# Kernel optimization log

Measured on AMD Instinct MI355X. Metric: run time of the kernel, lower is better.

## Reference

```python
import jax, jax.numpy as jnp
import numpy as np
from jax import lax

B, S, H, DK = 8192, 12, 8, 64
DM = H * DK  # d_model = 512


def setup_inputs() -> dict:
    key = jax.random.key(0)
    ks = jax.random.split(key, 7)
    query = jax.random.normal(ks[0], (B, S, DM), jnp.float32)
    key_t = jax.random.normal(ks[1], (B, S, DM), jnp.float32)
    value = jax.random.normal(ks[2], (B, S, DM), jnp.float32)
    mask = jnp.ones((B, S, S), jnp.int32)
    # conv1d12: Conv1d(12, 12, 3, 1, 1) -> weight [out_ch=12, in_ch=12, k=3]
    conv_w = jax.random.normal(ks[3], (S, S, 3), jnp.float32) * 0.1
    conv_b = jax.random.normal(ks[4], (S,), jnp.float32) * 0.1
    # final output projection linears[-1]: Linear(512, 512)
    W_out = jax.random.normal(ks[5], (DM, DM), jnp.float32) * (1.0 / np.sqrt(DM))
    b_out = jax.random.normal(ks[6], (DM,), jnp.float32) * 0.01
    return {"query": query, "key": key_t, "value": value, "mask": mask,
            "conv_w": conv_w, "conv_b": conv_b, "W_out": W_out, "b_out": b_out}


def _neighbor_sums(nodes):
    # nodes: [H, B, S, DK]. convo12 pattern == 3-tap sum over head index with zero ends:
    #   s0 = n0+n1; s_i = n_{i-1}+n_i+n_{i+1} (i=1..6); s7 = n6+n7
    p = jnp.pad(nodes, ((1, 1), (0, 0), (0, 0), (0, 0)))
    return p[:-2] + p[1:-1] + p[2:]  # [H, B, S, DK]


def _conv12(x, w, b):
    # x: [N, S, DK] -> conv over length DK with S channels, kernel 3, pad 1
    y = lax.conv_general_dilated(x, w, window_strides=(1,), padding=[(1, 1)],
                                 dimension_numbers=("NCH", "OIH", "NCH"))
    return y + b[None, :, None]


def reference(query, key, value, mask, conv_w, conv_b, W_out, b_out):
    def split_heads(x):
        # torch.split(x, d_k, -1) over 8 heads -> [H, B, S, DK]
        return jnp.moveaxis(x.reshape(B, S, H, DK), 2, 0)

    def conv_all(x):
        s = _neighbor_sums(split_heads(x)).reshape(H * B, S, DK)
        return _conv12(s, conv_w, conv_b).reshape(H, B, S, DK)

    # reunion: stack heads at dim 1 -> [B, H, S, DK]
    q = jnp.moveaxis(conv_all(query), 0, 1)
    k = jnp.moveaxis(conv_all(key), 0, 1)
    v = jnp.moveaxis(conv_all(value), 0, 1)

    scores = jnp.einsum("bhqd,bhkd->bhqk", q, k) / np.sqrt(DK).astype(np.float32)
    # mask.unsqueeze(1): [B,1,S,S]; masked_fill(mask==0, -1e9)
    scores = jnp.where(mask[:, None, :, :] == 0, jnp.float32(-1e9), scores)
    p = jax.nn.softmax(scores, axis=-1)  # dropout = identity (eval mode)
    x = jnp.einsum("bhqk,bhkd->bhqd", p, v)
    x = jnp.moveaxis(x, 1, 2).reshape(B, S, DM)  # transpose(1,2).view
    return x @ W_out.T + b_out
```

## Files before the change

kernel.cpp:

```cpp
#include <hip/hip_runtime.h>
#include <hip/hip_bf16.h>
#include <math.h>

#define NB 8192
#define NS 12
#define NH 8
#define NDK 64
#define NDM 512

typedef __attribute__((ext_vector_type(8))) short bf16x8;
typedef __attribute__((ext_vector_type(4))) float f32x4;

static __device__ __forceinline__ short f2bfb(float x) {
    __hip_bfloat16 h = __float2bfloat16(x);
    return *(short*)&h;
}
static __device__ __forceinline__ float bfb2f(short s) {
    unsigned u = ((unsigned)(unsigned short)s) << 16;
    return __uint_as_float(u);
}

__global__ __launch_bounds__(512) void wcvt_kernel(const float* __restrict__ W,
                                                   __hip_bfloat16* __restrict__ Wb) {
    int i = blockIdx.x * 512 + threadIdx.x;
    Wb[i] = __float2bfloat16(W[i]);
}

__global__ __launch_bounds__(256) void conv4_kernel(
    const float* __restrict__ gq, const float* __restrict__ gk, const float* __restrict__ gv,
    const float* __restrict__ gcw, const float* __restrict__ gcb,
    short* __restrict__ qc, short* __restrict__ kc, short* __restrict__ vc)
{
    __shared__ __align__(16) float wt[3][12][12];
    __shared__ __align__(16) float bconv[12];

    const int tid = threadIdx.x;
    for (int i = tid; i < 444; i += 256) {
        if (i < 432) {
            int t = i / 144, rem = i - t * 144;
            int s2 = rem / 12, s = rem - s2 * 12;
            wt[t][s2][s] = gcw[s * 36 + s2 * 3 + t];
        } else {
            bconv[i - 432] = gcb[i - 432];
        }
    }
    __syncthreads();

    const int t3   = blockIdx.y;
    const int lane = tid & 63;
    const int w    = tid >> 6;
    const int d4   = lane & 15;
    const int d0   = d4 * 4;
    const int h    = ((w & 1) << 2) + (lane >> 4);
    const int b    = blockIdx.x * 2 + (w >> 1);

    const float* src = (t3 == 0) ? gq : (t3 == 1) ? gk : gv;
    const float* xb  = src + (size_t)b * (NS * NDM);

    const float fm = (h > 0) ? 1.f : 0.f;
    const float fp = (h < 7) ? 1.f : 0.f;
    const float4* pa = (const float4*)(xb + h * 64 + d0);
    const float4* pm = (const float4*)(xb + (h > 0 ? h - 1 : h) * 64 + d0);
    const float4* pp = (const float4*)(xb + (h < 7 ? h + 1 : h) * 64 + d0);

    f32x4 o[12];
    #pragma unroll
    for (int s = 0; s < 12; ++s) {
        float bs = bconv[s];
        o[s] = (f32x4){bs, bs, bs, bs};
    }

    #pragma unroll 2
    for (int s2 = 0; s2 < 12; ++s2) {
        float4 a  = pa[s2 * 128];
        float4 am = pm[s2 * 128];
        float4 ap = pp[s2 * 128];
        f32x4 ns;
        ns[0] = a.x + am.x * fm + ap.x * fp;
        ns[1] = a.y + am.y * fm + ap.y * fp;
        ns[2] = a.z + am.z * fm + ap.z * fp;
        ns[3] = a.w + am.w * fm + ap.w * fp;

        float prev = __shfl_up(ns[3], 1, 16);   if (d4 == 0)  prev = 0.f;
        float next = __shfl_down(ns[0], 1, 16); if (d4 == 15) next = 0.f;
        f32x4 nsm = {prev, ns[0], ns[1], ns[2]};
        f32x4 nsp = {ns[1], ns[2], ns[3], next};

        #pragma unroll
        for (int tap = 0; tap < 3; ++tap) {
            const f32x4 nv = (tap == 0) ? nsm : (tap == 1) ? ns : nsp;
            #pragma unroll
            for (int G = 0; G < 3; ++G) {
                f32x4 wv = *(const f32x4*)&wt[tap][s2][G * 4];
                o[G * 4 + 0] += nv * wv[0];
                o[G * 4 + 1] += nv * wv[1];
                o[G * 4 + 2] += nv * wv[2];
                o[G * 4 + 3] += nv * wv[3];
            }
        }
    }

    if (t3 < 2) {
        short* dst = ((t3 == 0) ? qc : kc) + ((size_t)b * NH + h) * (NS * NDK) + d0;
        #pragma unroll
        for (int s = 0; s < 12; ++s) {
            short4 v;
            v.x = f2bfb(o[s][0]); v.y = f2bfb(o[s][1]);
            v.z = f2bfb(o[s][2]); v.w = f2bfb(o[s][3]);
            *(short4*)(dst + s * 64) = v;
        }
    } else {
        short* dstb = vc + (((size_t)b * NH + h) * NDK + d0) * NS;
        #pragma unroll
        for (int dd = 0; dd < 4; ++dd) {
            short4* dst = (short4*)(dstb + dd * NS);
            short4 p0, p1, p2;
            p0.x = f2bfb(o[0][dd]); p0.y = f2bfb(o[1][dd]); p0.z = f2bfb(o[2][dd]);  p0.w = f2bfb(o[3][dd]);
            p1.x = f2bfb(o[4][dd]); p1.y = f2bfb(o[5][dd]); p1.z = f2bfb(o[6][dd]);  p1.w = f2bfb(o[7][dd]);
            p2.x = f2bfb(o[8][dd]); p2.y = f2bfb(o[9][dd]); p2.z = f2bfb(o[10][dd]); p2.w = f2bfb(o[11][dd]);
            dst[0] = p0; dst[1] = p1; dst[2] = p2;
        }
    }
}

__global__ __launch_bounds__(512) void attn3_kernel(
    const short* __restrict__ qc, const short* __restrict__ kc, const short* __restrict__ vc,
    const int* __restrict__ gmask, const __hip_bfloat16* __restrict__ Wb,
    const float* __restrict__ gbo, float* __restrict__ gout)
{
    __shared__ __align__(16) short abuf[48 * 520];
    __shared__ __align__(16) short pbuf[NH][16][24];

    const int tid = threadIdx.x;
    const int w   = tid >> 6;
    const int ln  = tid & 63;
    const int rA  = ln & 15, g = ln >> 4;

    const int b0    = blockIdx.x * 4;
    const int bb    = w & 3;
    const int b     = b0 + bb;
    const int hbase = (w >> 2) * 4;

    const int rAr = (rA < 12) ? rA : 0;

    for (int t = 0; t < 4; ++t) {
        const int h = hbase + t;
        const short* qs = qc + ((size_t)b * NH + h) * (NS * NDK);
        const short* ks = kc + ((size_t)b * NH + h) * (NS * NDK);
        bf16x8 aq0 = *(const bf16x8*)(qs + rAr * 64 + g * 8);
        bf16x8 aq1 = *(const bf16x8*)(qs + rAr * 64 + 32 + g * 8);
        bf16x8 bk0 = *(const bf16x8*)(ks + rAr * 64 + g * 8);
        bf16x8 bk1 = *(const bf16x8*)(ks + rAr * 64 + 32 + g * 8);
        f32x4 sc = {0.f, 0.f, 0.f, 0.f};
        sc = __builtin_amdgcn_mfma_f32_16x16x32_bf16(aq0, bk0, sc, 0, 0, 0);
        sc = __builtin_amdgcn_mfma_f32_16x16x32_bf16(aq1, bk1, sc, 0, 0, 0);

        const int kj = rA;
        const int* mrow = gmask + (size_t)b * 144;
        #pragma unroll
        for (int r = 0; r < 4; ++r) {
            int qi = g * 4 + r;
            float s = sc[r] * 0.125f;
            if (kj >= 12) s = -INFINITY;
            else if (qi < 12 && mrow[qi * 12 + kj] == 0) s = -1e9f;
            float m = s;
            #pragma unroll
            for (int off = 1; off < 16; off <<= 1) m = fmaxf(m, __shfl_xor(m, off, 16));
            float e = __expf(s - m);
            float sum = e;
            #pragma unroll
            for (int off = 1; off < 16; off <<= 1) sum += __shfl_xor(sum, off, 16);
            pbuf[w][qi][kj] = f2bfb(e / sum);
        }

        bf16x8 pa = (bf16x8){0, 0, 0, 0, 0, 0, 0, 0};
        if (g < 2) pa = *(const bf16x8*)(&pbuf[w][rA][g * 8]);

        const short* vcr = vc + (((size_t)b * NH + h) * NDK) * NS;
        #pragma unroll
        for (int i = 0; i < 4; ++i) {
            bf16x8 bv = (bf16x8){0, 0, 0, 0, 0, 0, 0, 0};
            if (g < 2) {
                const short* p = vcr + (i * 16 + rA) * NS + g * 8;
                short4 lo = *(const short4*)(p);
                short4 hi = *(const short4*)(p + 4);
                bv[0] = lo.x; bv[1] = lo.y; bv[2] = lo.z; bv[3] = lo.w;
                bv[4] = hi.x; bv[5] = hi.y; bv[6] = hi.z; bv[7] = hi.w;
            }
            f32x4 pv = {0.f, 0.f, 0.f, 0.f};
            pv = __builtin_amdgcn_mfma_f32_16x16x32_bf16(pa, bv, pv, 0, 0, 0);
            #pragma unroll
            for (int r = 0; r < 4; ++r) {
                int qi = g * 4 + r;
                if (qi < 12)
                    abuf[(bb * 12 + qi) * 520 + h * 64 + i * 16 + rA] = f2bfb(pv[r]);
            }
        }
    }
    __syncthreads();

    {
        const short* Ws = (const short*)Wb;
        const int n_lane = w * 64 + rA;
        f32x4 acc[3][4] = {};
        #pragma unroll 4
        for (int kk = 0; kk < 16; ++kk) {
            int k0 = kk * 32 + g * 8;
            bf16x8 af0 = *(const bf16x8*)(abuf + (rA)      * 520 + k0);
            bf16x8 af1 = *(const bf16x8*)(abuf + (16 + rA) * 520 + k0);
            bf16x8 af2 = *(const bf16x8*)(abuf + (32 + rA) * 520 + k0);
            #pragma unroll
            for (int i = 0; i < 4; ++i) {
                bf16x8 bfg = *(const bf16x8*)(Ws + (size_t)(n_lane + i * 16) * NDM + k0);
                acc[0][i] = __builtin_amdgcn_mfma_f32_16x16x32_bf16(af0, bfg, acc[0][i], 0, 0, 0);
                acc[1][i] = __builtin_amdgcn_mfma_f32_16x16x32_bf16(af1, bfg, acc[1][i], 0, 0, 0);
                acc[2][i] = __builtin_amdgcn_mfma_f32_16x16x32_bf16(af2, bfg, acc[2][i], 0, 0, 0);
            }
        }
        float bias[4];
        #pragma unroll
        for (int i = 0; i < 4; ++i) bias[i] = gbo[w * 64 + i * 16 + rA];
        #pragma unroll
        for (int m = 0; m < 3; ++m) {
            #pragma unroll
            for (int i = 0; i < 4; ++i) {
                int n = w * 64 + i * 16 + rA;
                #pragma unroll
                for (int r = 0; r < 4; ++r) {
                    int mg  = m * 16 + g * 4 + r;
                    int bi  = mg / 12, qi = mg - bi * 12;
                    gout[(((size_t)(b0 + bi)) * NS + qi) * NDM + n] = acc[m][i][r] + bias[i];
                }
            }
        }
    }
}

__global__ __launch_bounds__(512) void mha_fused4_kernel(
    const float* __restrict__ gq, const float* __restrict__ gk, const float* __restrict__ gv,
    const int* __restrict__ gmask, const float* __restrict__ gcw, const float* __restrict__ gcb,
    const __hip_bfloat16* __restrict__ Wb, const float* __restrict__ gbo,
    float* __restrict__ gout)
{
    __shared__ __align__(16) float xstage[NS][NDM];
    __shared__ __align__(16) short ovbuf[18432];
    __shared__ __align__(16) float probs[NH][16][16];
    __shared__ __align__(16) float wt[3][12][12];
    __shared__ __align__(16) float bconv[12];

    const int b   = blockIdx.x;
    const int tid = threadIdx.x;
    const int wv  = tid >> 6;
    const int ln  = tid & 63;
    const int h = wv, d = ln;

    if (tid < 432) {
        int t = tid / 144, rem = tid - t * 144;
        int s2 = rem / 12, s = rem - s2 * 12;
        wt[t][s2][s] = gcw[s * 36 + s2 * 3 + t];
    } else if (tid < 444) {
        bconv[tid - 432] = gcb[tid - 432];
    }

    const size_t xoff = (size_t)b * (NS * NDM);
    float vv[12];

    for (int t3 = 0; t3 < 3; ++t3) {
        const float* xb = ((t3 == 0) ? gq : (t3 == 1) ? gk : gv) + xoff;
        {
            const float4* s4 = (const float4*)xb;
            float4* dst4 = (float4*)&xstage[0][0];
            #pragma unroll
            for (int i = 0; i < 3; ++i) dst4[tid + i * 512] = s4[tid + i * 512];
        }
        __syncthreads();

        f32x4 o0 = *(const f32x4*)&bconv[0];
        f32x4 o1 = *(const f32x4*)&bconv[4];
        f32x4 o2 = *(const f32x4*)&bconv[8];
        #pragma unroll 4
        for (int s2 = 0; s2 < 12; ++s2) {
            float c  = xstage[s2][h * 64 + d];
            float cm = (h > 0) ? xstage[s2][(h - 1) * 64 + d] : 0.f;
            float cp = (h < 7) ? xstage[s2][(h + 1) * 64 + d] : 0.f;
            float n0 = c + cm + cp;
            float nm = __shfl_up(n0, 1);   if (d == 0)  nm = 0.f;
            float np = __shfl_down(n0, 1); if (d == 63) np = 0.f;
            const f32x4* w0 = (const f32x4*)&wt[0][s2][0];
            const f32x4* w1 = (const f32x4*)&wt[1][s2][0];
            const f32x4* w2 = (const f32x4*)&wt[2][s2][0];
            o0 += w0[0] * nm + w1[0] * n0 + w2[0] * np;
            o1 += w0[1] * nm + w1[1] * n0 + w2[1] * np;
            o2 += w0[2] * nm + w1[2] * n0 + w2[2] * np;
        }
        if (t3 < 2) {
            __hip_bfloat16* st = (__hip_bfloat16*)(ovbuf + (wv * 2 + t3) * 1152);
            #pragma unroll
            for (int s = 0; s < 4; ++s) st[s * 72 + d]       = __float2bfloat16(o0[s]);
            #pragma unroll
            for (int s = 0; s < 4; ++s) st[(s + 4) * 72 + d] = __float2bfloat16(o1[s]);
            #pragma unroll
            for (int s = 0; s < 4; ++s) st[(s + 8) * 72 + d] = __float2bfloat16(o2[s]);
            __syncthreads();
        } else {
            #pragma unroll
            for (int s = 0; s < 4; ++s) { vv[s] = o0[s]; vv[s + 4] = o1[s]; vv[s + 8] = o2[s]; }
        }
    }

    const short* qsp = ovbuf + (wv * 2 + 0) * 1152;
    const short* ksp = ovbuf + (wv * 2 + 1) * 1152;
    const int rA = ln & 15, g = ln >> 4;
    bf16x8 aq0 = *(const bf16x8*)(qsp + rA * 72 + g * 8);
    bf16x8 aq1 = *(const bf16x8*)(qsp + rA * 72 + 32 + g * 8);
    bf16x8 bk0 = *(const bf16x8*)(ksp + rA * 72 + g * 8);
    bf16x8 bk1 = *(const bf16x8*)(ksp + rA * 72 + 32 + g * 8);
    f32x4 sc = {0.f, 0.f, 0.f, 0.f};
    sc = __builtin_amdgcn_mfma_f32_16x16x32_bf16(aq0, bk0, sc, 0, 0, 0);
    sc = __builtin_amdgcn_mfma_f32_16x16x32_bf16(aq1, bk1, sc, 0, 0, 0);

    const int kj = rA;
    const int* mrow = gmask + (size_t)b * 144;
    #pragma unroll
    for (int r = 0; r < 4; ++r) {
        int qi = g * 4 + r;
        float s = sc[r] * 0.125f;
        if (kj >= 12) s = -INFINITY;
        else if (qi < 12 && mrow[qi * 12 + kj] == 0) s = -1e9f;
        float m = s;
        #pragma unroll
        for (int off = 1; off < 16; off <<= 1) m = fmaxf(m, __shfl_xor(m, off, 16));
        float e = __expf(s - m);
        float sum = e;
        #pragma unroll
        for (int off = 1; off < 16; off <<= 1) sum += __shfl_xor(sum, off, 16);
        probs[wv][qi][kj] = e / sum;
    }

    __syncthreads();

    __hip_bfloat16* ab = (__hip_bfloat16*)ovbuf;
    #pragma unroll
    for (int qi = 0; qi < 12; ++qi) {
        const f32x4* pr = (const f32x4*)&probs[wv][qi][0];
        f32x4 p0 = pr[0], p1 = pr[1], p2 = pr[2];
        float acc = 0.f;
        #pragma unroll
        for (int j = 0; j < 4; ++j) acc += p0[j] * vv[j] + p1[j] * vv[j + 4] + p2[j] * vv[j + 8];
        ab[qi * 520 + h * 64 + d] = __float2bfloat16(acc);
    }
    {
        unsigned* az = (unsigned*)(ovbuf + 12 * 520);
        for (int i = tid; i < 1040; i += 512) az[i] = 0u;
    }
    __syncthreads();

    {
        const short* Ws = (const short*)Wb;
        const short* As = ovbuf;
        f32x4 acc[4] = {};
        const int n_lane = wv * 64 + rA;
        #pragma unroll 4
        for (int kk = 0; kk < 16; ++kk) {
            int k0 = kk * 32 + g * 8;
            bf16x8 af = *(const bf16x8*)(As + rA * 520 + k0);
            #pragma unroll
            for (int i = 0; i < 4; ++i) {
                bf16x8 bfg = *(const bf16x8*)(Ws + (size_t)(n_lane + i * 16) * NDM + k0);
                acc[i] = __builtin_amdgcn_mfma_f32_16x16x32_bf16(af, bfg, acc[i], 0, 0, 0);
            }
        }
        float* outb = gout + (size_t)b * (NS * NDM);
        const int m0 = g * 4;
        #pragma unroll
        for (int i = 0; i < 4; ++i) {
            int n = wv * 64 + i * 16 + rA;
            float bias = gbo[n];
            #pragma unroll
            for (int r = 0; r < 4; ++r) {
                int m = m0 + r;
                if (m < 12) outb[m * NDM + n] = acc[i][r] + bias;
            }
        }
    }
}

extern "C" void kernel_launch(void* const* d_in, const int* in_sizes, int n_in,
                              void* d_out, int out_size, void* d_ws, size_t ws_size,
                              hipStream_t stream) {
    const float* q    = (const float*)d_in[0];
    const float* k    = (const float*)d_in[1];
    const float* v    = (const float*)d_in[2];
    const int*   mask = (const int*)d_in[3];
    const float* cw   = (const float*)d_in[4];
    const float* cb   = (const float*)d_in[5];
    const float* W    = (const float*)d_in[6];
    const float* bo   = (const float*)d_in[7];

    const size_t TEN = (size_t)NB * NH * NS * NDK * sizeof(short);
    const size_t REQ = 3 * TEN + (size_t)NDM * NDM * sizeof(short);

    if (ws_size >= REQ) {
        short* vc = (short*)d_ws;
        short* qc = vc + TEN / sizeof(short);
        short* kc = qc + TEN / sizeof(short);
        __hip_bfloat16* Wb = (__hip_bfloat16*)(kc + TEN / sizeof(short));

        hipLaunchKernelGGL(wcvt_kernel, dim3(512), dim3(512), 0, stream, W, Wb);
        hipLaunchKernelGGL(conv4_kernel, dim3(NB / 2, 3), dim3(256), 0, stream,
                           q, k, v, cw, cb, qc, kc, vc);
        hipLaunchKernelGGL(attn3_kernel, dim3(NB / 4), dim3(512), 0, stream,
                           qc, kc, vc, mask, Wb, bo, (float*)d_out);
    } else {
        __hip_bfloat16* Wb = (__hip_bfloat16*)d_ws;
        hipLaunchKernelGGL(wcvt_kernel, dim3(512), dim3(512), 0, stream, W, Wb);
        hipLaunchKernelGGL(mha_fused4_kernel, dim3(NB), dim3(512), 0, stream,
                           q, k, v, mask, cw, cb, Wb, bo, (float*)d_out);
    }
}
```

Baseline: 444.8 us.

## Split fused attention+projection into separate attention and projection kernels

Replaces the fused attention-plus-output-projection kernel with two kernels. One computes per-batch attention with one head per wave and writes bf16 attention output to workspace, and the other runs the 512x512 projection over 4 batches per block. This aims to give each stage its own parallel layout and avoid the serial per-head loop in the fused kernel. In exchange it adds an extra bf16 intermediate write and read in global memory, needs more workspace, and adds a kernel launch.

```diff
diff --git a/kernel.cpp b/kernel.cpp
--- a/kernel.cpp
+++ b/kernel.cpp
@@ -123,6 +123,144 @@
     }
 }
 
+__global__ __launch_bounds__(512) void attn4_kernel(
+    const short* __restrict__ qc, const short* __restrict__ kc, const short* __restrict__ vc,
+    const int* __restrict__ gmask, short* __restrict__ ao)
+{
+    __shared__ __align__(16) short obuf[12 * 512];
+    __shared__ __align__(16) short pbuf[NH][16][24];
+
+    const int tid = threadIdx.x;
+    const int w   = tid >> 6;
+    const int ln  = tid & 63;
+    const int rA  = ln & 15, g = ln >> 4;
+
+    const int b = blockIdx.x;
+    const int h = w;
+    const int rAr = (rA < 12) ? rA : 0;
+
+    const short* qs = qc + ((size_t)b * NH + h) * (NS * NDK);
+    const short* ks = kc + ((size_t)b * NH + h) * (NS * NDK);
+    bf16x8 aq0 = *(const bf16x8*)(qs + rAr * 64 + g * 8);
+    bf16x8 aq1 = *(const bf16x8*)(qs + rAr * 64 + 32 + g * 8);
+    bf16x8 bk0 = *(const bf16x8*)(ks + rAr * 64 + g * 8);
+    bf16x8 bk1 = *(const bf16x8*)(ks + rAr * 64 + 32 + g * 8);
+    f32x4 sc = {0.f, 0.f, 0.f, 0.f};
+    sc = __builtin_amdgcn_mfma_f32_16x16x32_bf16(aq0, bk0, sc, 0, 0, 0);
+    sc = __builtin_amdgcn_mfma_f32_16x16x32_bf16(aq1, bk1, sc, 0, 0, 0);
+
+    const int kj = rA;
+    const int* mrow = gmask + (size_t)b * 144;
+    #pragma unroll
+    for (int r = 0; r < 4; ++r) {
+        int qi = g * 4 + r;
+        float s = sc[r] * 0.125f;
+        if (kj >= 12) s = -INFINITY;
+        else if (qi < 12 && mrow[qi * 12 + kj] == 0) s = -1e9f;
+        float m = s;
+        #pragma unroll
+        for (int off = 1; off < 16; off <<= 1) m = fmaxf(m, __shfl_xor(m, off, 16));
+        float e = __expf(s - m);
+        float sum = e;
+        #pragma unroll
+        for (int off = 1; off < 16; off <<= 1) sum += __shfl_xor(sum, off, 16);
+        pbuf[w][qi][kj] = f2bfb(e / sum);
+    }
+
+    bf16x8 pa = (bf16x8){0, 0, 0, 0, 0, 0, 0, 0};
+    if (g < 2) pa = *(const bf16x8*)(&pbuf[w][rA][g * 8]);
+
+    const short* vcr = vc + (((size_t)b * NH + h) * NDK) * NS;
+    #pragma unroll
+    for (int i = 0; i < 4; ++i) {
+        bf16x8 bv = (bf16x8){0, 0, 0, 0, 0, 0, 0, 0};
+        if (g < 2) {
+            const short* p = vcr + (i * 16 + rA) * NS + g * 8;
+            short4 lo = *(const short4*)(p);
+            short4 hi = *(const short4*)(p + 4);
+            bv[0] = lo.x; bv[1] = lo.y; bv[2] = lo.z; bv[3] = lo.w;
+            bv[4] = hi.x; bv[5] = hi.y; bv[6] = hi.z; bv[7] = hi.w;
+        }
+        f32x4 pv = {0.f, 0.f, 0.f, 0.f};
+        pv = __builtin_amdgcn_mfma_f32_16x16x32_bf16(pa, bv, pv, 0, 0, 0);
+        #pragma unroll
+        for (int r = 0; r < 4; ++r) {
+            int qi = g * 4 + r;
+            if (qi < 12)
+                obuf[qi * 512 + h * 64 + i * 16 + rA] = f2bfb(pv[r]);
+        }
+    }
+    __syncthreads();
+
+    {
+        short* dst = ao + (size_t)b * (NS * NDM);
+        #pragma unroll
+        for (int c = tid; c < 768; c += 512)
+            *(bf16x8*)(dst + c * 8) = *(const bf16x8*)(obuf + c * 8);
+    }
+}
+
+__global__ __launch_bounds__(512) void proj_kernel(
+    const short* __restrict__ ao, const __hip_bfloat16* __restrict__ Wb,
+    const float* __restrict__ gbo, float* __restrict__ gout)
+{
+    __shared__ __align__(16) short abuf[48 * 520];
+
+    const int tid = threadIdx.x;
+    const int w   = tid >> 6;
+    const int ln  = tid & 63;
+    const int rA  = ln & 15, g = ln >> 4;
+    const int b0  = blockIdx.x * 4;
+
+    {
+        const short* src = ao + (size_t)b0 * (NS * NDM);
+        #pragma unroll
+        for (int j = 0; j < 6; ++j) {
+            int c   = tid + j * 512;
+            int row = c >> 6;
+            int col = (c & 63) * 8;
+            *(bf16x8*)(abuf + row * 520 + col) = *(const bf16x8*)(src + c * 8);
+        }
+    }
+    __syncthreads();
+
+    {
+        const short* Ws = (const short*)Wb;
+        const int n_lane = w * 64 + rA;
+        f32x4 acc[3][4] = {};
+        #pragma unroll 4
+        for (int kk = 0; kk < 16; ++kk) {
+            int k0 = kk * 32 + g * 8;
+            bf16x8 af0 = *(const bf16x8*)(abuf + (rA)      * 520 + k0);
+            bf16x8 af1 = *(const bf16x8*)(abuf + (16 + rA) * 520 + k0);
+            bf16x8 af2 = *(const bf16x8*)(abuf + (32 + rA) * 520 + k0);
+            #pragma unroll
+            for (int i = 0; i < 4; ++i) {
+                bf16x8 bfg = *(const bf16x8*)(Ws + (size_t)(n_lane + i * 16) * NDM + k0);
+                acc[0][i] = __builtin_amdgcn_mfma_f32_16x16x32_bf16(af0, bfg, acc[0][i], 0, 0, 0);
+                acc[1][i] = __builtin_amdgcn_mfma_f32_16x16x32_bf16(af1, bfg, acc[1][i], 0, 0, 0);
+                acc[2][i] = __builtin_amdgcn_mfma_f32_16x16x32_bf16(af2, bfg, acc[2][i], 0, 0, 0);
+            }
+        }
+        float bias[4];
+        #pragma unroll
+        for (int i = 0; i < 4; ++i) bias[i] = gbo[w * 64 + i * 16 + rA];
+        #pragma unroll
+        for (int m = 0; m < 3; ++m) {
+            #pragma unroll
+            for (int i = 0; i < 4; ++i) {
+                int n = w * 64 + i * 16 + rA;
+                #pragma unroll
+                for (int r = 0; r < 4; ++r) {
+                    int mg  = m * 16 + g * 4 + r;
+                    int bi  = mg / 12, qi = mg - bi * 12;
+                    gout[(((size_t)(b0 + bi)) * NS + qi) * NDM + n] = acc[m][i][r] + bias[i];
+                }
+            }
+        }
+    }
+}
+
 __global__ __launch_bounds__(512) void attn3_kernel(
     const short* __restrict__ qc, const short* __restrict__ kc, const short* __restrict__ vc,
     const int* __restrict__ gmask, const __hip_bfloat16* __restrict__ Wb,
@@ -140,7 +278,6 @@
     const int bb    = w & 3;
     const int b     = b0 + bb;
     const int hbase = (w >> 2) * 4;
-
     const int rAr = (rA < 12) ? rA : 0;
 
     for (int t = 0; t < 4; ++t) {
@@ -397,10 +534,26 @@
     const float* W    = (const float*)d_in[6];
     const float* bo   = (const float*)d_in[7];
 
-    const size_t TEN = (size_t)NB * NH * NS * NDK * sizeof(short);
-    const size_t REQ = 3 * TEN + (size_t)NDM * NDM * sizeof(short);
-
-    if (ws_size >= REQ) {
+    const size_t TEN  = (size_t)NB * NH * NS * NDK * sizeof(short);
+    const size_t WBS  = (size_t)NDM * NDM * sizeof(short);
+    const size_t REQ4 = 4 * TEN + WBS;
+    const size_t REQ3 = 3 * TEN + WBS;
+
+    if (ws_size >= REQ4) {
+        short* vc = (short*)d_ws;
+        short* qc = vc + TEN / sizeof(short);
+        short* kc = qc + TEN / sizeof(short);
+        short* ao = kc + TEN / sizeof(short);
+        __hip_bfloat16* Wb = (__hip_bfloat16*)(ao + TEN / sizeof(short));
+
+        hipLaunchKernelGGL(wcvt_kernel, dim3(512), dim3(512), 0, stream, W, Wb);
+        hipLaunchKernelGGL(conv4_kernel, dim3(NB / 2, 3), dim3(256), 0, stream,
+                           q, k, v, cw, cb, qc, kc, vc);
+        hipLaunchKernelGGL(attn4_kernel, dim3(NB), dim3(512), 0, stream,
+                           qc, kc, vc, mask, ao);
+        hipLaunchKernelGGL(proj_kernel, dim3(NB / 4), dim3(512), 0, stream,
+                           ao, Wb, bo, (float*)d_out);
+    } else if (ws_size >= REQ3) {
         short* vc = (short*)d_ws;
         short* qc = vc + TEN / sizeof(short);
         short* kc = qc + TEN / sizeof(short);
```

Result: no change. 447.5 us (+0.6%).
